# Kernel optimization log

Measured on AMD Instinct MI355X. Metric: run time of the kernel, lower is better.

The kernel has to match this reference:

```python
import jax, jax.numpy as jnp
import numpy as np

B, S, D = 4, 2048, 1024

def setup_inputs() -> dict:
    key = jax.random.key(0)
    kx, kq, kk, kv = jax.random.split(key, 4)
    scale = 0.02
    return {
        'x': jax.random.normal(kx, (B, S, D), dtype=jnp.float32),
        'wq': jax.random.normal(kq, (D, D), dtype=jnp.float32) * scale,
        'wk': jax.random.normal(kk, (D, D), dtype=jnp.float32) * scale,
        'wv': jax.random.normal(kv, (D, D), dtype=jnp.float32) * scale,
    }

def reference(x, wq, wk, wv):
    # QKV projections (no bias): nn.Linear applies x @ W^T; here wq is already [d_in, d_out]
    q = jnp.einsum('bsd,de->bse', x, wq)
    k = jnp.einsum('bsd,de->bse', x, wk)
    v = jnp.einsum('bsd,de->bse', x, wv)
    d_k = k.shape[-1]
    scores = jnp.einsum('bqd,bkd->bqk', q, k) / jnp.sqrt(jnp.float32(d_k))
    s = x.shape[1]
    causal = jnp.tril(jnp.ones((s, s), dtype=bool))  # True = keep
    scores = jnp.where(causal[None, :, :], scores, -jnp.inf)
    attn = jax.nn.softmax(scores, axis=-1)
    # dropout p=0.0 -> identity
    return jnp.einsum('bqk,bkd->bqd', attn, v)
```

## Files before the change

### kernel.cpp

```cpp
#include <hip/hip_runtime.h>
#include <hip/hip_bf16.h>


typedef __attribute__((ext_vector_type(8))) short bf16x8;
typedef __attribute__((ext_vector_type(4))) float f32x4;

#define GLOAD_LDS16(g, l)                                                     \
    __builtin_amdgcn_global_load_lds(                                         \
        (const __attribute__((address_space(1))) void*)(g),                   \
        (__attribute__((address_space(3))) void*)(l), 16, 0, 0)

__device__ __forceinline__ short f2bf(float f) {
    union { float f; unsigned u; } v; v.f = f;
    unsigned r = v.u + 0x7FFFu + ((v.u >> 16) & 1u);
    return (short)(r >> 16);
}

__global__ __launch_bounds__(256) void convx(const float* __restrict__ x,
                                             short* __restrict__ xb, int n4) {
    int i = blockIdx.x * 256 + threadIdx.x;
    if (i < n4) {
        float4 v = ((const float4*)x)[i];
        short4 o;
        o.x = f2bf(v.x); o.y = f2bf(v.y); o.z = f2bf(v.z); o.w = f2bf(v.w);
        ((short4*)xb)[i] = o;
    }
}

__global__ __launch_bounds__(256) void wtrans(const float* __restrict__ W,
                                              short* __restrict__ O) {
    int n0 = blockIdx.x * 64, k0 = blockIdx.y * 64;
    __shared__ float tile[64][65];
    int t = threadIdx.x;
#pragma unroll
    for (int i = 0; i < 16; ++i) {
        int idx = t + i * 256;
        int r = idx >> 6, c = idx & 63;
        tile[r][c] = W[(size_t)(k0 + r) * 1024 + n0 + c];
    }
    __syncthreads();
#pragma unroll
    for (int i = 0; i < 16; ++i) {
        int idx = t + i * 256;
        int r = idx >> 6, c = idx & 63;
        O[(size_t)(n0 + r) * 1024 + k0 + c] = f2bf(tile[c][r]);
    }
}

template <int MODE>
__global__ __launch_bounds__(256, 2) void gemm128(
    const short* __restrict__ A0, int lda0, long long sA,
    const short* __restrict__ B0, int ldb0, long long sB,
    void* __restrict__ C0, float scale,
    const short* __restrict__ Av, const short* __restrict__ Bv,
    short* __restrict__ Cv) {

    int m0, n0, z = 0, lda = lda0, ldb = ldb0;
    const short* Ab;
    const short* Bb;
    bool isVT = false;

    if (MODE == 2) {
        int i = blockIdx.x;
        int j = i & 255;
        int mt = (i < 256) ? (15 - (j >> 5)) : (j >> 5);
        z = (j >> 3) & 3;
        m0 = mt * 128;
        n0 = (j & 7) * 128;
        Ab = A0 + (size_t)z * sA;
        Bb = B0 + (size_t)z * sB;
    } else {
        const int nblk = gridDim.x;
        const int raw = blockIdx.x;
        int bid = (raw & 7) * (nblk >> 3) + (raw >> 3);
        if (MODE == 5) {
            m0 = (bid >> 3) * 128;
            n0 = (bid & 7) * 128;
            Ab = A0; Bb = B0;
        } else {
            if (bid < 544) {
                z = bid / 136;
                int f = bid - z * 136;
                int mt = (int)((sqrtf(8.f * f + 1.f) - 1.f) * 0.5f);
                if (mt * (mt + 1) / 2 > f) --mt;
                if ((mt + 1) * (mt + 2) / 2 <= f) ++mt;
                int nt_ = f - mt * (mt + 1) / 2;
                m0 = mt * 128; n0 = nt_ * 128;
                Ab = A0 + (size_t)z * sA;
                Bb = B0 + (size_t)z * sB;
            } else {
                isVT = true;
                int v = bid - 544;
                m0 = (v >> 6) * 128;
                n0 = (v & 63) * 128;
                Ab = Av; Bb = Bv; lda = 1024; ldb = 1024;
            }
        }
    }

    const int tid = threadIdx.x;
    const int lane = tid & 63;
    const int wid = tid >> 6;
    const int wm = wid >> 1, wn = wid & 1;

    __shared__ __align__(16) short As[2][8192];
    __shared__ __align__(16) short Bs[2][8192];

    f32x4 acc[4][4] = {};

    const int Kend = (MODE == 2) ? (m0 + 128) : 1024;
    const int nt = Kend >> 6;

    const int srow = tid >> 3;
    const int sl = (tid & 7) ^ (srow & 7);
    const short* Agp = Ab + (size_t)(m0 + srow) * lda + sl * 8;
    const short* Bgp = Bb + (size_t)(n0 + srow) * ldb + sl * 8;

#define SA(kt, bf)                                                            \
    do {                                                                      \
        const int _k = (kt) << 6;                                             \
        GLOAD_LDS16(Agp + _k,                     &As[bf][tid * 8]);          \
        GLOAD_LDS16(Agp + _k + (size_t)32 * lda,  &As[bf][2048 + tid * 8]);   \
        GLOAD_LDS16(Agp + _k + (size_t)64 * lda,  &As[bf][4096 + tid * 8]);   \
        GLOAD_LDS16(Agp + _k + (size_t)96 * lda,  &As[bf][6144 + tid * 8]);   \
    } while (0)
#define SB(kt, bf)                                                            \
    do {                                                                      \
        const int _k = (kt) << 6;                                             \
        GLOAD_LDS16(Bgp + _k,                     &Bs[bf][tid * 8]);          \
        GLOAD_LDS16(Bgp + _k + (size_t)32 * ldb,  &Bs[bf][2048 + tid * 8]);   \
        GLOAD_LDS16(Bgp + _k + (size_t)64 * ldb,  &Bs[bf][4096 + tid * 8]);   \
        GLOAD_LDS16(Bgp + _k + (size_t)96 * ldb,  &Bs[bf][6144 + tid * 8]);   \
    } while (0)

    const int r = lane & 15;
    const int g = lane >> 4;

#define LDA4(dst, bf, kk)                                                     \
    _Pragma("unroll") for (int q = 0; q < 4; ++q) {                           \
        const int rr = wm * 64 + q * 16 + r;                                  \
        dst[q] = *(const bf16x8*)&As[bf][rr * 64 +                            \
                                         ((((kk)*4 + g) ^ (rr & 7))) * 8];    \
    }
#define LDB4(dst, bf, kk)                                                     \
    _Pragma("unroll") for (int q = 0; q < 4; ++q) {                           \
        const int rb = wn * 64 + q * 16 + r;                                  \
        dst[q] = *(const bf16x8*)&Bs[bf][rb * 64 +                            \
                                         ((((kk)*4 + g) ^ (rb & 7))) * 8];    \
    }
#define LGKM0()                                                               \
    asm volatile("s_waitcnt lgkmcnt(0)" ::: "memory");                        \
    __builtin_amdgcn_sched_barrier(0)
#define VM0() asm volatile("s_waitcnt vmcnt(0)" ::: "memory")
#define BAR() __builtin_amdgcn_s_barrier()
#define MF(ar, br)                                                            \
    _Pragma("unroll") for (int mi = 0; mi < 4; ++mi)                          \
        _Pragma("unroll") for (int ni = 0; ni < 4; ++ni)                      \
            acc[mi][ni] = __builtin_amdgcn_mfma_f32_16x16x32_bf16(            \
                ar[mi], br[ni], acc[mi][ni], 0, 0, 0);

    SA(0, 0); SB(0, 0);
    VM0();
    BAR();

    int buf = 0;
    for (int t = 0; t < nt - 1; ++t) {
        const int nb = buf ^ 1;
        SA(t + 1, nb); SB(t + 1, nb);
        bf16x8 a[4], b[4];
        LDA4(a, buf, 0); LDB4(b, buf, 0);
        LGKM0();
        MF(a, b);
        LDA4(a, buf, 1); LDB4(b, buf, 1);
        LGKM0();
        MF(a, b);
        VM0();
        BAR();
        buf = nb;
    }
    {
        bf16x8 a[4], b[4];
        LDA4(a, buf, 0); LDB4(b, buf, 0);
        LGKM0();
        MF(a, b);
        LDA4(a, buf, 1); LDB4(b, buf, 1);
        LGKM0();
        MF(a, b);
    }

    const int r4 = (lane >> 4) * 4;
#pragma unroll
    for (int mi = 0; mi < 4; ++mi) {
#pragma unroll
        for (int ni = 0; ni < 4; ++ni) {
            int col = n0 + wn * 64 + ni * 16 + r;
#pragma unroll
            for (int i = 0; i < 4; ++i) {
                int rr = m0 + wm * 64 + mi * 16 + r4 + i;
                float v = acc[mi][ni][i];
                if (MODE == 5) {
                    ((short*)C0)[(size_t)rr * 1024 + col] = f2bf(v * scale);
                } else if (MODE == 1) {
                    if (isVT) {
                        Cv[(size_t)(col >> 11) * 2097152 +
                           (size_t)rr * 2048 + (col & 2047)] = f2bf(v);
                    } else if (col <= rr) {
                        ((float*)C0)[(size_t)z * 4194304 +
                                     (size_t)rr * 2048 + col] = v;
                    }
                } else {
                    ((float*)C0)[(size_t)z * 2097152 +
                                 (size_t)rr * 1024 + col] = v;
                }
            }
        }
    }
#undef SA
#undef SB
#undef LDA4
#undef LDB4
#undef LGKM0
#undef VM0
#undef BAR
#undef MF
}

__global__ __launch_bounds__(256) void softmax_causal(float* __restrict__ scores) {
    int row = blockIdx.x;
    int b = row >> 11, i = row & 2047;
    float* srow = scores + ((size_t)b * 2048 + i) * 2048;
    short* arow = (short*)srow;
    __shared__ float4 sv4[512];
    __shared__ float red[8];
    int t = threadIdx.x;
    int L = i + 1;
    int nv = (L + 3) >> 2;

    float mx = -1e30f;
    for (int v = t; v < nv; v += 256) {
        float4 w = ((const float4*)srow)[v];
        int base = v << 2;
        w.x = (base + 0 < L) ? w.x : -1e30f;
        w.y = (base + 1 < L) ? w.y : -1e30f;
        w.z = (base + 2 < L) ? w.z : -1e30f;
        w.w = (base + 3 < L) ? w.w : -1e30f;
        sv4[v] = w;
        mx = fmaxf(mx, fmaxf(fmaxf(w.x, w.y), fmaxf(w.z, w.w)));
    }
#pragma unroll
    for (int o = 32; o > 0; o >>= 1) mx = fmaxf(mx, __shfl_down(mx, o));
    if ((t & 63) == 0) red[t >> 6] = mx;
    __syncthreads();
    mx = fmaxf(fmaxf(red[0], red[1]), fmaxf(red[2], red[3]));

    float sum = 0.f;
    for (int v = t; v < nv; v += 256) {
        float4 w = sv4[v];
        float4 e;
        e.x = __expf(w.x - mx);
        e.y = __expf(w.y - mx);
        e.z = __expf(w.z - mx);
        e.w = __expf(w.w - mx);
        sv4[v] = e;
        sum += (e.x + e.y) + (e.z + e.w);
    }
#pragma unroll
    for (int o = 32; o > 0; o >>= 1) sum += __shfl_down(sum, o);
    if ((t & 63) == 0) red[4 + (t >> 6)] = sum;
    __syncthreads();
    sum = red[4] + red[5] + red[6] + red[7];
    float rinv = 1.0f / sum;

    int npad = ((i | 127) + 1) >> 2;
    for (int v = t; v < npad; v += 256) {
        float4 w = (v < nv) ? sv4[v] : float4{0.f, 0.f, 0.f, 0.f};
        short4 o4;
        o4.x = f2bf(w.x * rinv);
        o4.y = f2bf(w.y * rinv);
        o4.z = f2bf(w.z * rinv);
        o4.w = f2bf(w.w * rinv);
        ((short4*)arow)[v] = o4;
    }
}

extern "C" void kernel_launch(void* const* d_in, const int* in_sizes, int n_in,
                              void* d_out, int out_size, void* d_ws, size_t ws_size,
                              hipStream_t stream) {
    const float* x  = (const float*)d_in[0];
    const float* wq = (const float*)d_in[1];
    const float* wk = (const float*)d_in[2];
    const float* wv = (const float*)d_in[3];
    float* out = (float*)d_out;

    short* ws16 = (short*)d_ws;
    short* xb  = ws16;
    short* wqb = xb + 8388608;
    short* wkb = wqb + 1048576;
    short* wtv = wkb + 1048576;
    short* Mt  = wtv + 1048576;
    short* tb  = Mt + 1048576;
    short* vt  = tb + 8388608;
    float* scores = (float*)(vt + 8388608);

    convx<<<8192, 256, 0, stream>>>(x, xb, 2097152);
    convx<<<1024, 256, 0, stream>>>(wq, wqb, 262144);
    convx<<<1024, 256, 0, stream>>>(wk, wkb, 262144);
    wtrans<<<dim3(16, 16, 1), 256, 0, stream>>>(wv, wtv);
    gemm128<5><<<64, 256, 0, stream>>>(
        wkb, 1024, 0LL, wqb, 1024, 0LL, Mt, 0.03125f,
        nullptr, nullptr, nullptr);
    gemm128<5><<<512, 256, 0, stream>>>(
        xb, 1024, 0LL, Mt, 1024, 0LL, tb, 1.0f,
        nullptr, nullptr, nullptr);
    gemm128<1><<<1056, 256, 0, stream>>>(
        tb, 1024, 2097152LL, xb, 1024, 2097152LL, scores, 1.0f,
        wtv, xb, vt);
    softmax_causal<<<8192, 256, 0, stream>>>(scores);
    gemm128<2><<<512, 256, 0, stream>>>(
        (const short*)scores, 4096, 8388608LL, vt, 2048, 2097152LL, out, 1.0f,
        nullptr, nullptr, nullptr);
}
```

Baseline: 171.4 us.

## Store scores in bf16, wave-per-row softmax, fuse conversions, overlap LDS reads

The score GEMM now writes bf16 instead of fp32, which halves score traffic. Softmax now runs one wavefront per row with register-resident values instead of LDS and block barriers. The three fp32-to-bf16 conversion launches become a single kernel. The GEMM inner loop issues both k-slices of LDS reads before waiting, so the first MFMA batch can start after a partial lgkmcnt. Rounding the scores to bf16 before softmax loses some precision, and holding both k-slices raises register pressure.

```diff
diff --git a/kernel.cpp b/kernel.cpp
--- a/kernel.cpp
+++ b/kernel.cpp
@@ -15,15 +15,30 @@
     unsigned r = v.u + 0x7FFFu + ((v.u >> 16) & 1u);
     return (short)(r >> 16);
 }
-
-__global__ __launch_bounds__(256) void convx(const float* __restrict__ x,
-                                             short* __restrict__ xb, int n4) {
+__device__ __forceinline__ float bf2f(short h) {
+    union { unsigned u; float f; } v;
+    v.u = ((unsigned)(unsigned short)h) << 16;
+    return v.f;
+}
+
+__global__ __launch_bounds__(256) void convall(
+    const float* __restrict__ x, const float* __restrict__ wq,
+    const float* __restrict__ wk, short* __restrict__ xb,
+    short* __restrict__ wqb, short* __restrict__ wkb) {
     int i = blockIdx.x * 256 + threadIdx.x;
-    if (i < n4) {
-        float4 v = ((const float4*)x)[i];
+#pragma unroll
+    for (int s = 0; s < 5; ++s) {
+        int v = i + s * 524288;
+        const float* src;
+        short* dst;
+        int off;
+        if (v < 2097152)      { src = x;  dst = xb;  off = v; }
+        else if (v < 2359296) { src = wq; dst = wqb; off = v - 2097152; }
+        else                  { src = wk; dst = wkb; off = v - 2359296; }
+        float4 w = ((const float4*)src)[off];
         short4 o;
-        o.x = f2bf(v.x); o.y = f2bf(v.y); o.z = f2bf(v.z); o.w = f2bf(v.w);
-        ((short4*)xb)[i] = o;
+        o.x = f2bf(w.x); o.y = f2bf(w.y); o.z = f2bf(w.z); o.w = f2bf(w.w);
+        ((short4*)dst)[off] = o;
     }
 }
 
@@ -148,8 +163,8 @@
         dst[q] = *(const bf16x8*)&Bs[bf][rb * 64 +                            \
                                          ((((kk)*4 + g) ^ (rb & 7))) * 8];    \
     }
-#define LGKM0()                                                               \
-    asm volatile("s_waitcnt lgkmcnt(0)" ::: "memory");                        \
+#define LGKM(n)                                                               \
+    asm volatile("s_waitcnt lgkmcnt(" #n ")" ::: "memory");                   \
     __builtin_amdgcn_sched_barrier(0)
 #define VM0() asm volatile("s_waitcnt vmcnt(0)" ::: "memory")
 #define BAR() __builtin_amdgcn_s_barrier()
@@ -167,25 +182,27 @@
     for (int t = 0; t < nt - 1; ++t) {
         const int nb = buf ^ 1;
         SA(t + 1, nb); SB(t + 1, nb);
-        bf16x8 a[4], b[4];
-        LDA4(a, buf, 0); LDB4(b, buf, 0);
-        LGKM0();
-        MF(a, b);
-        LDA4(a, buf, 1); LDB4(b, buf, 1);
-        LGKM0();
-        MF(a, b);
+        bf16x8 a0[4], b0[4], a1[4], b1[4];
+        LDA4(a0, buf, 0); LDB4(b0, buf, 0);
+        __builtin_amdgcn_sched_barrier(0);
+        LDA4(a1, buf, 1); LDB4(b1, buf, 1);
+        LGKM(8);
+        MF(a0, b0);
+        LGKM(0);
+        MF(a1, b1);
         VM0();
         BAR();
         buf = nb;
     }
     {
-        bf16x8 a[4], b[4];
-        LDA4(a, buf, 0); LDB4(b, buf, 0);
-        LGKM0();
-        MF(a, b);
-        LDA4(a, buf, 1); LDB4(b, buf, 1);
-        LGKM0();
-        MF(a, b);
+        bf16x8 a0[4], b0[4], a1[4], b1[4];
+        LDA4(a0, buf, 0); LDB4(b0, buf, 0);
+        __builtin_amdgcn_sched_barrier(0);
+        LDA4(a1, buf, 1); LDB4(b1, buf, 1);
+        LGKM(8);
+        MF(a0, b0);
+        LGKM(0);
+        MF(a1, b1);
     }
 
     const int r4 = (lane >> 4) * 4;
@@ -205,8 +222,8 @@
                         Cv[(size_t)(col >> 11) * 2097152 +
                            (size_t)rr * 2048 + (col & 2047)] = f2bf(v);
                     } else if (col <= rr) {
-                        ((float*)C0)[(size_t)z * 4194304 +
-                                     (size_t)rr * 2048 + col] = v;
+                        ((short*)C0)[(size_t)z * 4194304 +
+                                     (size_t)rr * 2048 + col] = f2bf(v);
                     }
                 } else {
                     ((float*)C0)[(size_t)z * 2097152 +
@@ -219,67 +236,65 @@
 #undef SB
 #undef LDA4
 #undef LDB4
-#undef LGKM0
+#undef LGKM
 #undef VM0
 #undef BAR
 #undef MF
 }
 
-__global__ __launch_bounds__(256) void softmax_causal(float* __restrict__ scores) {
-    int row = blockIdx.x;
+__global__ __launch_bounds__(256) void softmax_wave(short* __restrict__ scores) {
+    int row = (blockIdx.x << 2) + (threadIdx.x >> 6);
+    int lane = threadIdx.x & 63;
     int b = row >> 11, i = row & 2047;
-    float* srow = scores + ((size_t)b * 2048 + i) * 2048;
-    short* arow = (short*)srow;
-    __shared__ float4 sv4[512];
-    __shared__ float red[8];
-    int t = threadIdx.x;
+    short* srow = scores + ((size_t)(b << 11) + i) * 2048;
     int L = i + 1;
-    int nv = (L + 3) >> 2;
-
+    int Lpad = (i | 127) + 1;
+
+    float vals[32];
     float mx = -1e30f;
-    for (int v = t; v < nv; v += 256) {
-        float4 w = ((const float4*)srow)[v];
-        int base = v << 2;
-        w.x = (base + 0 < L) ? w.x : -1e30f;
-        w.y = (base + 1 < L) ? w.y : -1e30f;
-        w.z = (base + 2 < L) ? w.z : -1e30f;
-        w.w = (base + 3 < L) ? w.w : -1e30f;
-        sv4[v] = w;
-        mx = fmaxf(mx, fmaxf(fmaxf(w.x, w.y), fmaxf(w.z, w.w)));
+#pragma unroll
+    for (int s = 0; s < 4; ++s) {
+        if (s * 512 < Lpad) {
+            int j0 = (s << 9) + (lane << 3);
+            bf16x8 h = *(const bf16x8*)&srow[j0];
+#pragma unroll
+            for (int e = 0; e < 8; ++e) {
+                float f = ((j0 + e) < L) ? bf2f(h[e]) : -1e30f;
+                vals[s * 8 + e] = f;
+                mx = fmaxf(mx, f);
+            }
+        }
     }
 #pragma unroll
     for (int o = 32; o > 0; o >>= 1) mx = fmaxf(mx, __shfl_down(mx, o));
-    if ((t & 63) == 0) red[t >> 6] = mx;
-    __syncthreads();
-    mx = fmaxf(fmaxf(red[0], red[1]), fmaxf(red[2], red[3]));
+    mx = __shfl(mx, 0);
 
     float sum = 0.f;
-    for (int v = t; v < nv; v += 256) {
-        float4 w = sv4[v];
-        float4 e;
-        e.x = __expf(w.x - mx);
-        e.y = __expf(w.y - mx);
-        e.z = __expf(w.z - mx);
-        e.w = __expf(w.w - mx);
-        sv4[v] = e;
-        sum += (e.x + e.y) + (e.z + e.w);
+#pragma unroll
+    for (int s = 0; s < 4; ++s) {
+        if (s * 512 < Lpad) {
+#pragma unroll
+            for (int e = 0; e < 8; ++e) {
+                float ex = __expf(vals[s * 8 + e] - mx);
+                vals[s * 8 + e] = ex;
+                sum += ex;
+            }
+        }
     }
 #pragma unroll
     for (int o = 32; o > 0; o >>= 1) sum += __shfl_down(sum, o);
-    if ((t & 63) == 0) red[4 + (t >> 6)] = sum;
-    __syncthreads();
-    sum = red[4] + red[5] + red[6] + red[7];
+    sum = __shfl(sum, 0);
     float rinv = 1.0f / sum;
 
-    int npad = ((i | 127) + 1) >> 2;
-    for (int v = t; v < npad; v += 256) {
-        float4 w = (v < nv) ? sv4[v] : float4{0.f, 0.f, 0.f, 0.f};
-        short4 o4;
-        o4.x = f2bf(w.x * rinv);
-        o4.y = f2bf(w.y * rinv);
-        o4.z = f2bf(w.z * rinv);
-        o4.w = f2bf(w.w * rinv);
-        ((short4*)arow)[v] = o4;
+#pragma unroll
+    for (int s = 0; s < 4; ++s) {
+        if (s * 512 < Lpad) {
+            int j0 = (s << 9) + (lane << 3);
+            bf16x8 o8;
+#pragma unroll
+            for (int e = 0; e < 8; ++e) o8[e] = f2bf(vals[s * 8 + e] * rinv);
+            *(bf16x8*)&srow[j0] = o8;
+        }
     }
 }
 
@@ -300,11 +315,9 @@
     short* Mt  = wtv + 1048576;
     short* tb  = Mt + 1048576;
     short* vt  = tb + 8388608;
-    float* scores = (float*)(vt + 8388608);
-
-    convx<<<8192, 256, 0, stream>>>(x, xb, 2097152);
-    convx<<<1024, 256, 0, stream>>>(wq, wqb, 262144);
-    convx<<<1024, 256, 0, stream>>>(wk, wkb, 262144);
+    short* scores = vt + 8388608;
+
+    convall<<<2048, 256, 0, stream>>>(x, wq, wk, xb, wqb, wkb);
     wtrans<<<dim3(16, 16, 1), 256, 0, stream>>>(wv, wtv);
     gemm128<5><<<64, 256, 0, stream>>>(
         wkb, 1024, 0LL, wqb, 1024, 0LL, Mt, 0.03125f,
@@ -315,8 +328,8 @@
     gemm128<1><<<1056, 256, 0, stream>>>(
         tb, 1024, 2097152LL, xb, 1024, 2097152LL, scores, 1.0f,
         wtv, xb, vt);
-    softmax_causal<<<8192, 256, 0, stream>>>(scores);
+    softmax_wave<<<2048, 256, 0, stream>>>(scores);
     gemm128<2><<<512, 256, 0, stream>>>(
-        (const short*)scores, 4096, 8388608LL, vt, 2048, 2097152LL, out, 1.0f,
+        scores, 2048, 4194304LL, vt, 2048, 2097152LL, out, 1.0f,
         nullptr, nullptr, nullptr);
 }
```

Result: faster. 164.1 us (-4.3%).
